# Kernel optimization log

Measured on AMD Instinct MI355X. Metric: run time of the kernel, lower is better.

The kernel has to match this reference:

```python
import math
import jax, jax.numpy as jnp
import numpy as np

B, S, D, H, M, R = 4, 2048, 512, 8, 4, 32
HD = D // H
EPS = 1e-8


def setup_inputs() -> dict:
    key = jax.random.key(0)
    ks = jax.random.split(key, 12)
    sc = 1.0 / math.sqrt(D)
    return {
        "x": jax.random.normal(ks[0], (B, S, D), jnp.float32),
        "Wq": jax.random.normal(ks[1], (D, D), jnp.float32) * sc,
        "bq": jnp.zeros((D,), jnp.float32),
        "Wk": jax.random.normal(ks[2], (D, D), jnp.float32) * sc,
        "bk": jnp.zeros((D,), jnp.float32),
        "Wv": jax.random.normal(ks[3], (D, D), jnp.float32) * sc,
        "bv": jnp.zeros((D,), jnp.float32),
        "mask1": jax.random.normal(ks[4], (M, R, S), jnp.float32) * (1.0 / math.sqrt(R)),
        "mask2": jax.random.normal(ks[5], (M, R, S), jnp.float32) * (1.0 / math.sqrt(R)),
        "Wo": jax.random.normal(ks[6], (D, D), jnp.float32) * sc,
        "bo": jnp.zeros((D,), jnp.float32),
        "roll_back": jax.random.randint(ks[7], (1, S, S), 0, S, jnp.int32),
    }


def reference(x, Wq, bq, Wk, bk, Wv, bv, mask1, mask2, Wo, bo, roll_back):
    # q, k, v: [B, H, S, HD]  (torch Linear: x @ W.T + b)
    def proj(W, b):
        return (x @ W.T + b).reshape(B, S, H, HD).transpose(0, 2, 1, 3)
    q, k, v = proj(Wq, bq), proj(Wk, bk), proj(Wv, bv)

    # learnable_mask[m,s,t] = sum_r mask1[m,r,s] * mask2[m,r,t]  -> [M, S, S]
    lm = jnp.einsum("mrs,mrt->mst", mask1, mask2)
    # gather along last dim with roll indices expanded to [M, S, S]
    idx = jnp.broadcast_to(roll_back, lm.shape)
    lm_rolled = jnp.take_along_axis(lm, idx, axis=-1)  # [M, S, S]

    # att: [B, H, S, S]
    att = jnp.einsum("bhsd,bhtd->bhst", q, k) / math.sqrt(HD)
    # group heads: [B, H/M, M, S, S] * [1, 1, M, S, S]
    att = att.reshape(B, H // M, M, S, S) * lm_rolled[None, None]
    att = att.reshape(B, H, S, S)

    # Frobenius norm over last two dims, per (batch, head)
    fro = jnp.sqrt(jnp.sum(att * att, axis=(-2, -1), keepdims=True))
    att = att / (fro + EPS)

    out = jnp.einsum("bhst,bhtd->bshd", att, v).reshape(B, S, D)
    return out @ Wo.T + bo
```

## Files before the change

### kernel.cpp

```cpp
#include <hip/hip_runtime.h>
#include <hip/hip_bf16.h>

#define NB 4
#define NS 2048
#define ND 512
#define NH 8
#define NM 4
#define NR 32
#define NHD 64

typedef short frag_ab __attribute__((ext_vector_type(8)));
typedef float frag_cd __attribute__((ext_vector_type(4)));

__device__ __forceinline__ float bf2f(short s) {
    union { unsigned u; float f; } c;
    c.u = ((unsigned)(unsigned short)s) << 16;
    return c.f;
}
__device__ __forceinline__ short f2bf(float f) {
    __hip_bfloat16 h = __float2bfloat16(f);
    union { __hip_bfloat16 h; short s; } c;
    c.h = h;
    return c.s;
}

__device__ __forceinline__ void gload16(const void* g, void* l) {
    __builtin_amdgcn_global_load_lds((const __attribute__((address_space(1))) unsigned int*)g,
                                     (__attribute__((address_space(3))) unsigned int*)l,
                                     16, 0, 0);
}

__device__ __forceinline__ void stage_tile(const short* src, size_t srcStride,
                                           char* lbase, int slot) {
    int o = slot * 16;
    int row = o >> 7;
    int cc = ((o >> 4) & 7) ^ (row & 7);
    gload16(src + (size_t)row * srcStride + cc * 8, lbase + o);
}

__device__ __forceinline__ frag_ab lds_frag(const char* lbase, int row, int cc_un) {
    int cc = cc_un ^ (row & 7);
    return *(const frag_ab*)(lbase + row * 128 + cc * 16);
}

__global__ void __launch_bounds__(256) k_cast(const float* __restrict__ in,
                                              short* __restrict__ out, int n8) {
    int i = blockIdx.x * 256 + threadIdx.x;
    if (i >= n8) return;
    const float4* p = (const float4*)in + (size_t)i * 2;
    float4 a = p[0], b = p[1];
    frag_ab o;
    o[0] = f2bf(a.x); o[1] = f2bf(a.y); o[2] = f2bf(a.z); o[3] = f2bf(a.w);
    o[4] = f2bf(b.x); o[5] = f2bf(b.y); o[6] = f2bf(b.z); o[7] = f2bf(b.w);
    ((frag_ab*)out)[i] = o;
}

__global__ void __launch_bounds__(256) k_tcast_mask(const float* __restrict__ in,
                                                    short* __restrict__ out) {
    int m = blockIdx.y, s0 = blockIdx.x * 64, tid = threadIdx.x;
    __shared__ float tile[32][65];
    int c = tid & 63, r4 = tid >> 6;
#pragma unroll
    for (int p = 0; p < 8; ++p) {
        int r = p * 4 + r4;
        tile[r][c] = in[(m * 32 + r) * NS + s0 + c];
    }
    __syncthreads();
    int r = tid & 31, s4 = tid >> 5;
#pragma unroll
    for (int p = 0; p < 8; ++p) {
        int s = p * 8 + s4;
        out[(m * NS + s0 + s) * NR + r] = f2bf(tile[r][s]);
    }
}

__global__ void __launch_bounds__(64) k_lm(const short* __restrict__ m1t,
                                           const short* __restrict__ m2t,
                                           short* __restrict__ lm) {
    int tb = blockIdx.x * 64, sb = blockIdx.y * 64, m = blockIdx.z;
    int lane = threadIdx.x;
    int lo = lane & 15, g = lane >> 4;
    frag_ab a[4], b[4];
#pragma unroll
    for (int i = 0; i < 4; ++i) {
        a[i] = *(const frag_ab*)(m1t + (m * NS + sb + i * 16 + lo) * NR + g * 8);
        b[i] = *(const frag_ab*)(m2t + (m * NS + tb + i * 16 + lo) * NR + g * 8);
    }
#pragma unroll
    for (int mi = 0; mi < 4; ++mi)
#pragma unroll
        for (int ni = 0; ni < 4; ++ni) {
            frag_cd z = {0.f, 0.f, 0.f, 0.f};
            frag_cd d = __builtin_amdgcn_mfma_f32_16x16x32_bf16(a[mi], b[ni], z, 0, 0, 0);
#pragma unroll
            for (int r = 0; r < 4; ++r) {
                int srow = sb + mi * 16 + g * 4 + r;
                int tcol = tb + ni * 16 + lo;
                lm[(size_t)(m * NS + srow) * NS + tcol] = f2bf(d[r]);
            }
        }
}

__global__ void __launch_bounds__(256) k_roll(const short* __restrict__ lm,
                                              const int* __restrict__ roll,
                                              short* __restrict__ lmr) {
    int bid = blockIdx.x;
    int m = bid & 3, s = bid >> 2;
    __shared__ __align__(16) short row[NS];
    int tid = threadIdx.x;
    size_t base = (size_t)(m * NS + s) * NS;
    *(frag_ab*)(row + tid * 8) = *(const frag_ab*)(lm + base + tid * 8);
    __syncthreads();
    const int* rrow = roll + (size_t)s * NS;
#pragma unroll
    for (int k = 0; k < 8; ++k) {
        int t = k * 256 + tid;
        lmr[base + t] = row[rrow[t]];
    }
}

template <int MODE>
__global__ void __launch_bounds__(256) k_gemm(const short* __restrict__ A,
                                              const short* __restrict__ W,
                                              const float* __restrict__ bias,
                                              void* __restrict__ out) {
    int n = blockIdx.x;
    int Mb = (n & 7) * 8 + ((n >> 3) & 7);
    int Nb = n >> 6;
    int bm0 = Mb * 128, bn0 = Nb * 128;
    int tid = threadIdx.x;
    int wid = tid >> 6, lane = tid & 63;
    int lo = lane & 15, g = lane >> 4;
    int wr = (wid >> 1) * 64, wc = (wid & 1) * 64;

    __shared__ __align__(16) char sm[2][32768];

    frag_cd acc[4][4];
#pragma unroll
    for (int mi = 0; mi < 4; ++mi)
#pragma unroll
        for (int ni = 0; ni < 4; ++ni) acc[mi][ni] = (frag_cd){0.f, 0.f, 0.f, 0.f};

    const short* Abase = A + (size_t)bm0 * ND;
    const short* Wbase = W + (size_t)bn0 * ND;

#pragma unroll
    for (int j = 0; j < 4; ++j) stage_tile(Abase, ND, sm[0], tid + j * 256);
#pragma unroll
    for (int j = 0; j < 4; ++j) stage_tile(Wbase, ND, sm[0] + 16384, tid + j * 256);
    __syncthreads();

    char* cb = sm[0];
    char* nb = sm[1];
    for (int kt = 0; kt < 8; ++kt) {
        if (kt < 7) {
            int k0 = (kt + 1) * 64;
#pragma unroll
            for (int j = 0; j < 4; ++j) stage_tile(Abase + k0, ND, nb, tid + j * 256);
#pragma unroll
            for (int j = 0; j < 4; ++j) stage_tile(Wbase + k0, ND, nb + 16384, tid + j * 256);
        }
#pragma unroll
        for (int kk = 0; kk < 2; ++kk) {
            frag_ab af[4], bf[4];
#pragma unroll
            for (int mi = 0; mi < 4; ++mi) af[mi] = lds_frag(cb, wr + mi * 16 + lo, kk * 4 + g);
#pragma unroll
            for (int ni = 0; ni < 4; ++ni) bf[ni] = lds_frag(cb + 16384, wc + ni * 16 + lo, kk * 4 + g);
#pragma unroll
            for (int mi = 0; mi < 4; ++mi)
#pragma unroll
                for (int ni = 0; ni < 4; ++ni)
                    acc[mi][ni] = __builtin_amdgcn_mfma_f32_16x16x32_bf16(af[mi], bf[ni], acc[mi][ni], 0, 0, 0);
        }
        __syncthreads();
        char* t = cb; cb = nb; nb = t;
    }

#pragma unroll
    for (int mi = 0; mi < 4; ++mi)
#pragma unroll
        for (int ni = 0; ni < 4; ++ni)
#pragma unroll
            for (int r = 0; r < 4; ++r) {
                int row = bm0 + wr + mi * 16 + g * 4 + r;
                int col = bn0 + wc + ni * 16 + lo;
                float v = acc[mi][ni][r] + bias[col];
                int b = row >> 11, s = row & 2047, h = col >> 6, d = col & 63;
                if (MODE == 0) {
                    ((short*)out)[(((size_t)(b * NH + h) * NS + s) << 6) + d] = f2bf(v);
                } else if (MODE == 1) {
                    ((short*)out)[((size_t)(b * NH + h) * NHD + d) * NS + s] = f2bf(v);
                } else {
                    ((float*)out)[(size_t)row * ND + col] = v;
                }
            }
}

__global__ void __launch_bounds__(512) k_attn(const short* __restrict__ Qb,
                                              const short* __restrict__ Kb,
                                              const short* __restrict__ Vt,
                                              const short* __restrict__ lmr,
                                              short* __restrict__ O,
                                              float* __restrict__ fro) {
    int n = blockIdx.x;
    int h = n & 7;
    int slot = n >> 3;
    int b = slot >> 4;
    int sb = slot & 15;
    int bh = b * NH + h;
    int m = h & 3;
    int tid = threadIdx.x;
    int w = tid >> 6, lane = tid & 63;
    int lo = lane & 15, g = lane >> 4;
    int srow = sb * 128 + w * 16;

    __shared__ __align__(16) char kv[2][16384];
    __shared__ __align__(16) short plds[8][1024];
    char* pbase = (char*)&plds[w][0];

    const short* kbase = Kb + (size_t)bh * NS * NHD;
    const short* vbase = Vt + (size_t)bh * NHD * NS;
    const short* lmbase = lmr + ((size_t)m * NS + srow + lo) * NS;

    const short* qptr = Qb + ((size_t)bh * NS + srow + lo) * NHD + g * 8;
    frag_ab qf[2];
    qf[0] = *(const frag_ab*)(qptr);
    qf[1] = *(const frag_ab*)(qptr + 32);

    frag_cd acco[4];
#pragma unroll
    for (int ni = 0; ni < 4; ++ni) acco[ni] = (frag_cd){0.f, 0.f, 0.f, 0.f};
    float sumsq = 0.f;

    stage_tile(kbase, NHD, kv[0], tid);
    stage_tile(vbase, NS, kv[0] + 8192, tid);
    __syncthreads();

    char* cb = kv[0];
    char* nb = kv[1];
    for (int tb = 0; tb < 32; ++tb) {
        int t0 = tb * 64;
        if (tb < 31) {
            stage_tile(kbase + (size_t)(t0 + 64) * NHD, NHD, nb, tid);
            stage_tile(vbase + (t0 + 64), NS, nb + 8192, tid);
        }
        frag_cd sacc[4];
#pragma unroll
        for (int ni = 0; ni < 4; ++ni) sacc[ni] = (frag_cd){0.f, 0.f, 0.f, 0.f};
#pragma unroll
        for (int kk = 0; kk < 2; ++kk)
#pragma unroll
            for (int ni = 0; ni < 4; ++ni)
                sacc[ni] = __builtin_amdgcn_mfma_f32_16x16x32_bf16(
                    qf[kk], lds_frag(cb, ni * 16 + lo, kk * 4 + g), sacc[ni], 0, 0, 0);
#pragma unroll
        for (int ni = 0; ni < 4; ++ni)
#pragma unroll
            for (int r = 0; r < 4; ++r) {
                int rs = g * 4 + r;
                int ct = ni * 16 + lo;
                int byte = (rs * 128 + ct * 2) ^ ((rs & 7) << 4);
                *(short*)(pbase + byte) = f2bf(sacc[ni][r]);
            }
        frag_ab pf[2];
#pragma unroll
        for (int kk = 0; kk < 2; ++kk) {
            int rbyte = (lo * 128 + kk * 64 + g * 16) ^ ((lo & 7) << 4);
            frag_ab sf = *(const frag_ab*)(pbase + rbyte);
            frag_ab lf = *(const frag_ab*)(lmbase + t0 + kk * 32 + g * 8);
            frag_ab pp;
#pragma unroll
            for (int j = 0; j < 8; ++j) {
                float p = bf2f(sf[j]) * bf2f(lf[j]) * 0.125f;
                sumsq += p * p;
                pp[j] = f2bf(p);
            }
            pf[kk] = pp;
        }
#pragma unroll
        for (int ni = 0; ni < 4; ++ni)
#pragma unroll
            for (int kk = 0; kk < 2; ++kk)
                acco[ni] = __builtin_amdgcn_mfma_f32_16x16x32_bf16(
                    pf[kk], lds_frag(cb + 8192, ni * 16 + lo, kk * 4 + g), acco[ni], 0, 0, 0);
        __syncthreads();
        char* t = cb; cb = nb; nb = t;
    }
#pragma unroll
    for (int off = 32; off; off >>= 1) sumsq += __shfl_xor(sumsq, off, 64);
    if (lane == 0) atomicAdd(&fro[bh], sumsq);
#pragma unroll
    for (int ni = 0; ni < 4; ++ni)
#pragma unroll
        for (int r = 0; r < 4; ++r) {
            int s = srow + g * 4 + r;
            int d = ni * 16 + lo;
            O[((size_t)(b * NS + s)) * ND + h * NHD + d] = f2bf(acco[ni][r]);
        }
}

__global__ void k_fro(const float* __restrict__ fro, float* __restrict__ inv) {
    int i = threadIdx.x;
    if (i < NB * NH) inv[i] = 1.f / (sqrtf(fro[i]) + 1e-8f);
}

__global__ void __launch_bounds__(256) k_scale(short* __restrict__ O,
                                               const float* __restrict__ inv) {
    int i = blockIdx.x * 256 + threadIdx.x;
    int i8 = i * 8;
    int col = i8 & 511;
    int row = i8 >> 9;
    float sc = inv[(row >> 11) * NH + (col >> 6)];
    frag_ab v = ((frag_ab*)O)[i];
    frag_ab o;
#pragma unroll
    for (int j = 0; j < 8; ++j) o[j] = f2bf(bf2f(v[j]) * sc);
    ((frag_ab*)O)[i] = o;
}

extern "C" void kernel_launch(void* const* d_in, const int* in_sizes, int n_in,
                              void* d_out, int out_size, void* d_ws, size_t ws_size,
                              hipStream_t stream) {
    const float* x     = (const float*)d_in[0];
    const float* Wq    = (const float*)d_in[1];
    const float* bq    = (const float*)d_in[2];
    const float* Wk    = (const float*)d_in[3];
    const float* bk    = (const float*)d_in[4];
    const float* Wv    = (const float*)d_in[5];
    const float* bv    = (const float*)d_in[6];
    const float* mask1 = (const float*)d_in[7];
    const float* mask2 = (const float*)d_in[8];
    const float* Wo    = (const float*)d_in[9];
    const float* bo    = (const float*)d_in[10];
    const int*   roll  = (const int*)d_in[11];
    float* out = (float*)d_out;

    char* ws = (char*)d_ws;
    short* xb  = (short*)(ws + 0);
    short* Wqb = (short*)(ws + 8388608);
    short* Wkb = (short*)(ws + 8912896);
    short* Wvb = (short*)(ws + 9437184);
    short* Wob = (short*)(ws + 9961472);
    short* Qb  = (short*)(ws + 10485760);
    short* Kb  = (short*)(ws + 18874368);
    short* Vtb = (short*)(ws + 27262976);
    short* m1t = (short*)(ws + 35651584);
    short* m2t = (short*)(ws + 36175872);
    short* lm  = (short*)(ws + 36700160);
    short* lmr = (short*)(ws + 70254592);
    short* Ob  = (short*)(ws + 103809024);
    float* fro = (float*)(ws + 112197632);
    float* inv = (float*)(ws + 112197760);

    k_cast<<<2048, 256, 0, stream>>>(x, xb, (NB * NS * ND) / 8);
    k_cast<<<128, 256, 0, stream>>>(Wq, Wqb, (ND * ND) / 8);
    k_cast<<<128, 256, 0, stream>>>(Wk, Wkb, (ND * ND) / 8);
    k_cast<<<128, 256, 0, stream>>>(Wv, Wvb, (ND * ND) / 8);
    k_cast<<<128, 256, 0, stream>>>(Wo, Wob, (ND * ND) / 8);
    k_tcast_mask<<<dim3(32, 4), 256, 0, stream>>>(mask1, m1t);
    k_tcast_mask<<<dim3(32, 4), 256, 0, stream>>>(mask2, m2t);

    k_lm<<<dim3(32, 32, 4), 64, 0, stream>>>(m1t, m2t, lm);
    k_roll<<<8192, 256, 0, stream>>>(lm, roll, lmr);

    k_gemm<0><<<256, 256, 0, stream>>>(xb, Wqb, bq, Qb);
    k_gemm<0><<<256, 256, 0, stream>>>(xb, Wkb, bk, Kb);
    k_gemm<1><<<256, 256, 0, stream>>>(xb, Wvb, bv, Vtb);

    hipMemsetAsync(fro, 0, 128, stream);
    k_attn<<<512, 512, 0, stream>>>(Qb, Kb, Vtb, lmr, Ob, fro);

    k_fro<<<1, 64, 0, stream>>>(fro, inv);
    k_scale<<<2048, 256, 0, stream>>>(Ob, inv);
    k_gemm<2><<<256, 256, 0, stream>>>(Ob, Wob, bo, out);
}
```

Before: 285.8 us.

## Merge launches, fuse QKV GEMMs, vectorize roll gather, prefetch mask, remap attention blocks

Measured after the change: 252.9 us. 11.5% less time.

```diff
diff --git a/kernel.cpp b/kernel.cpp
--- a/kernel.cpp
+++ b/kernel.cpp
@@ -55,9 +55,32 @@
     ((frag_ab*)out)[i] = o;
 }
 
-__global__ void __launch_bounds__(256) k_tcast_mask(const float* __restrict__ in,
-                                                    short* __restrict__ out) {
-    int m = blockIdx.y, s0 = blockIdx.x * 64, tid = threadIdx.x;
+__global__ void __launch_bounds__(256) k_castw(const float* __restrict__ Wq,
+                                               const float* __restrict__ Wk,
+                                               const float* __restrict__ Wv,
+                                               const float* __restrict__ Wo,
+                                               short* __restrict__ out) {
+    int i = blockIdx.x * 256 + threadIdx.x;
+    int which = i >> 15;
+    int j = i & 32767;
+    const float* src = which == 0 ? Wq : which == 1 ? Wk : which == 2 ? Wv : Wo;
+    const float4* p = (const float4*)src + (size_t)j * 2;
+    float4 a = p[0], b = p[1];
+    frag_ab o;
+    o[0] = f2bf(a.x); o[1] = f2bf(a.y); o[2] = f2bf(a.z); o[3] = f2bf(a.w);
+    o[4] = f2bf(b.x); o[5] = f2bf(b.y); o[6] = f2bf(b.z); o[7] = f2bf(b.w);
+    ((frag_ab*)out)[i] = o;
+}
+
+__global__ void __launch_bounds__(256) k_tcast_mask(const float* __restrict__ mask1,
+                                                    const float* __restrict__ mask2,
+                                                    short* __restrict__ m1t,
+                                                    short* __restrict__ m2t) {
+    int my = blockIdx.y;
+    const float* in = my < 4 ? mask1 : mask2;
+    short* out = my < 4 ? m1t : m2t;
+    int m = my & 3;
+    int s0 = blockIdx.x * 64, tid = threadIdx.x;
     __shared__ float tile[32][65];
     int c = tid & 63, r4 = tid >> 6;
 #pragma unroll
@@ -112,34 +135,47 @@
     *(frag_ab*)(row + tid * 8) = *(const frag_ab*)(lm + base + tid * 8);
     __syncthreads();
     const int* rrow = roll + (size_t)s * NS;
-#pragma unroll
-    for (int k = 0; k < 8; ++k) {
-        int t = k * 256 + tid;
-        lmr[base + t] = row[rrow[t]];
-    }
-}
-
-template <int MODE>
-__global__ void __launch_bounds__(256) k_gemm(const short* __restrict__ A,
-                                              const short* __restrict__ W,
-                                              const float* __restrict__ bias,
-                                              void* __restrict__ out) {
+    int t0 = tid * 8;
+    int4 r0 = *(const int4*)(rrow + t0);
+    int4 r1 = *(const int4*)(rrow + t0 + 4);
+    frag_ab o;
+    o[0] = row[r0.x]; o[1] = row[r0.y]; o[2] = row[r0.z]; o[3] = row[r0.w];
+    o[4] = row[r1.x]; o[5] = row[r1.y]; o[6] = row[r1.z]; o[7] = row[r1.w];
+    *(frag_ab*)(lmr + base + t0) = o;
+}
+
+__global__ void __launch_bounds__(256) k_gemm_qkv(const short* __restrict__ A,
+                                                  const short* __restrict__ Wqb,
+                                                  const short* __restrict__ Wkb,
+                                                  const short* __restrict__ Wvb,
+                                                  const float* __restrict__ bq,
+                                                  const float* __restrict__ bk,
+                                                  const float* __restrict__ bv,
+                                                  short* __restrict__ Qb,
+                                                  short* __restrict__ Kb,
+                                                  short* __restrict__ Vtb) {
     int n = blockIdx.x;
-    int Mb = (n & 7) * 8 + ((n >> 3) & 7);
-    int Nb = n >> 6;
-    int bm0 = Mb * 128, bn0 = Nb * 128;
+    int rr = n >> 3;
+    int Mb = (n & 7) * 8 + (rr & 7);
+    int Nb = rr >> 3;
+    int which = Nb >> 3;
+    int bn0 = (Nb & 7) * 64;
+    const short* W = which == 0 ? Wqb : which == 1 ? Wkb : Wvb;
+    const float* bias = which == 0 ? bq : which == 1 ? bk : bv;
+    short* out = which == 0 ? Qb : which == 1 ? Kb : Vtb;
+    int bm0 = Mb * 128;
     int tid = threadIdx.x;
     int wid = tid >> 6, lane = tid & 63;
     int lo = lane & 15, g = lane >> 4;
-    int wr = (wid >> 1) * 64, wc = (wid & 1) * 64;
-
-    __shared__ __align__(16) char sm[2][32768];
-
-    frag_cd acc[4][4];
+    int wr = (wid >> 1) * 64, wc = (wid & 1) * 32;
+
+    __shared__ __align__(16) char sm[2][24576];
+
+    frag_cd acc[4][2];
 #pragma unroll
     for (int mi = 0; mi < 4; ++mi)
 #pragma unroll
-        for (int ni = 0; ni < 4; ++ni) acc[mi][ni] = (frag_cd){0.f, 0.f, 0.f, 0.f};
+        for (int ni = 0; ni < 2; ++ni) acc[mi][ni] = (frag_cd){0.f, 0.f, 0.f, 0.f};
 
     const short* Abase = A + (size_t)bm0 * ND;
     const short* Wbase = W + (size_t)bn0 * ND;
@@ -147,7 +183,7 @@
 #pragma unroll
     for (int j = 0; j < 4; ++j) stage_tile(Abase, ND, sm[0], tid + j * 256);
 #pragma unroll
-    for (int j = 0; j < 4; ++j) stage_tile(Wbase, ND, sm[0] + 16384, tid + j * 256);
+    for (int j = 0; j < 2; ++j) stage_tile(Wbase, ND, sm[0] + 16384, tid + j * 256);
     __syncthreads();
 
     char* cb = sm[0];
@@ -158,19 +194,19 @@
 #pragma unroll
             for (int j = 0; j < 4; ++j) stage_tile(Abase + k0, ND, nb, tid + j * 256);
 #pragma unroll
-            for (int j = 0; j < 4; ++j) stage_tile(Wbase + k0, ND, nb + 16384, tid + j * 256);
+            for (int j = 0; j < 2; ++j) stage_tile(Wbase + k0, ND, nb + 16384, tid + j * 256);
         }
 #pragma unroll
         for (int kk = 0; kk < 2; ++kk) {
-            frag_ab af[4], bf[4];
+            frag_ab af[4], bf[2];
 #pragma unroll
             for (int mi = 0; mi < 4; ++mi) af[mi] = lds_frag(cb, wr + mi * 16 + lo, kk * 4 + g);
 #pragma unroll
-            for (int ni = 0; ni < 4; ++ni) bf[ni] = lds_frag(cb + 16384, wc + ni * 16 + lo, kk * 4 + g);
+            for (int ni = 0; ni < 2; ++ni) bf[ni] = lds_frag(cb + 16384, wc + ni * 16 + lo, kk * 4 + g);
 #pragma unroll
             for (int mi = 0; mi < 4; ++mi)
 #pragma unroll
-                for (int ni = 0; ni < 4; ++ni)
+                for (int ni = 0; ni < 2; ++ni)
                     acc[mi][ni] = __builtin_amdgcn_mfma_f32_16x16x32_bf16(af[mi], bf[ni], acc[mi][ni], 0, 0, 0);
         }
         __syncthreads();
@@ -180,20 +216,89 @@
 #pragma unroll
     for (int mi = 0; mi < 4; ++mi)
 #pragma unroll
-        for (int ni = 0; ni < 4; ++ni)
-#pragma unroll
-            for (int r = 0; r < 4; ++r) {
-                int row = bm0 + wr + mi * 16 + g * 4 + r;
+        for (int ni = 0; ni < 2; ++ni)
+#pragma unroll
+            for (int ri = 0; ri < 4; ++ri) {
+                int row = bm0 + wr + mi * 16 + g * 4 + ri;
                 int col = bn0 + wc + ni * 16 + lo;
-                float v = acc[mi][ni][r] + bias[col];
+                float v = acc[mi][ni][ri] + bias[col];
                 int b = row >> 11, s = row & 2047, h = col >> 6, d = col & 63;
-                if (MODE == 0) {
-                    ((short*)out)[(((size_t)(b * NH + h) * NS + s) << 6) + d] = f2bf(v);
-                } else if (MODE == 1) {
-                    ((short*)out)[((size_t)(b * NH + h) * NHD + d) * NS + s] = f2bf(v);
+                if (which < 2) {
+                    out[(((size_t)(b * NH + h) * NS + s) << 6) + d] = f2bf(v);
                 } else {
-                    ((float*)out)[(size_t)row * ND + col] = v;
+                    out[((size_t)(b * NH + h) * NHD + d) * NS + s] = f2bf(v);
                 }
+            }
+}
+
+__global__ void __launch_bounds__(256) k_gemm_out(const short* __restrict__ A,
+                                                  const short* __restrict__ W,
+                                                  const float* __restrict__ bias,
+                                                  float* __restrict__ out) {
+    int n = blockIdx.x;
+    int rr = n >> 3;
+    int Mb = (n & 7) * 8 + (rr & 7);
+    int Nb = rr >> 3;
+    int bn0 = Nb * 64;
+    int bm0 = Mb * 128;
+    int tid = threadIdx.x;
+    int wid = tid >> 6, lane = tid & 63;
+    int lo = lane & 15, g = lane >> 4;
+    int wr = (wid >> 1) * 64, wc = (wid & 1) * 32;
+
+    __shared__ __align__(16) char sm[2][24576];
+
+    frag_cd acc[4][2];
+#pragma unroll
+    for (int mi = 0; mi < 4; ++mi)
+#pragma unroll
+        for (int ni = 0; ni < 2; ++ni) acc[mi][ni] = (frag_cd){0.f, 0.f, 0.f, 0.f};
+
+    const short* Abase = A + (size_t)bm0 * ND;
+    const short* Wbase = W + (size_t)bn0 * ND;
+
+#pragma unroll
+    for (int j = 0; j < 4; ++j) stage_tile(Abase, ND, sm[0], tid + j * 256);
+#pragma unroll
+    for (int j = 0; j < 2; ++j) stage_tile(Wbase, ND, sm[0] + 16384, tid + j * 256);
+    __syncthreads();
+
+    char* cb = sm[0];
+    char* nb = sm[1];
+    for (int kt = 0; kt < 8; ++kt) {
+        if (kt < 7) {
+            int k0 = (kt + 1) * 64;
+#pragma unroll
+            for (int j = 0; j < 4; ++j) stage_tile(Abase + k0, ND, nb, tid + j * 256);
+#pragma unroll
+            for (int j = 0; j < 2; ++j) stage_tile(Wbase + k0, ND, nb + 16384, tid + j * 256);
+        }
+#pragma unroll
+        for (int kk = 0; kk < 2; ++kk) {
+            frag_ab af[4], bf[2];
+#pragma unroll
+            for (int mi = 0; mi < 4; ++mi) af[mi] = lds_frag(cb, wr + mi * 16 + lo, kk * 4 + g);
+#pragma unroll
+            for (int ni = 0; ni < 2; ++ni) bf[ni] = lds_frag(cb + 16384, wc + ni * 16 + lo, kk * 4 + g);
+#pragma unroll
+            for (int mi = 0; mi < 4; ++mi)
+#pragma unroll
+                for (int ni = 0; ni < 2; ++ni)
+                    acc[mi][ni] = __builtin_amdgcn_mfma_f32_16x16x32_bf16(af[mi], bf[ni], acc[mi][ni], 0, 0, 0);
+        }
+        __syncthreads();
+        char* t = cb; cb = nb; nb = t;
+    }
+
+#pragma unroll
+    for (int mi = 0; mi < 4; ++mi)
+#pragma unroll
+        for (int ni = 0; ni < 2; ++ni)
+#pragma unroll
+            for (int ri = 0; ri < 4; ++ri) {
+                int row = bm0 + wr + mi * 16 + g * 4 + ri;
+                int col = bn0 + wc + ni * 16 + lo;
+                out[(size_t)row * ND + col] = acc[mi][ni][ri] + bias[col];
             }
 }
 
@@ -204,12 +309,15 @@
                                               short* __restrict__ O,
                                               float* __restrict__ fro) {
     int n = blockIdx.x;
-    int h = n & 7;
-    int slot = n >> 3;
-    int b = slot >> 4;
-    int sb = slot & 15;
+    int xcd = n & 7;
+    int idx = n >> 3;
+    int b = idx & 3;
+    int hh = (idx >> 2) & 1;
+    int sbl = idx >> 3;
+    int m = xcd >> 1;
+    int sb = (xcd & 1) * 8 + sbl;
+    int h = hh * 4 + m;
     int bh = b * NH + h;
-    int m = h & 3;
     int tid = threadIdx.x;
     int w = tid >> 6, lane = tid & 63;
     int lo = lane & 15, g = lane >> 4;
@@ -235,15 +343,20 @@
 
     stage_tile(kbase, NHD, kv[0], tid);
     stage_tile(vbase, NS, kv[0] + 8192, tid);
+    frag_ab lc0 = *(const frag_ab*)(lmbase + g * 8);
+    frag_ab lc1 = *(const frag_ab*)(lmbase + 32 + g * 8);
     __syncthreads();
 
     char* cb = kv[0];
     char* nb = kv[1];
     for (int tb = 0; tb < 32; ++tb) {
         int t0 = tb * 64;
+        frag_ab ln0 = lc0, ln1 = lc1;
         if (tb < 31) {
             stage_tile(kbase + (size_t)(t0 + 64) * NHD, NHD, nb, tid);
             stage_tile(vbase + (t0 + 64), NS, nb + 8192, tid);
+            ln0 = *(const frag_ab*)(lmbase + t0 + 64 + g * 8);
+            ln1 = *(const frag_ab*)(lmbase + t0 + 96 + g * 8);
         }
         frag_cd sacc[4];
 #pragma unroll
@@ -268,7 +381,7 @@
         for (int kk = 0; kk < 2; ++kk) {
             int rbyte = (lo * 128 + kk * 64 + g * 16) ^ ((lo & 7) << 4);
             frag_ab sf = *(const frag_ab*)(pbase + rbyte);
-            frag_ab lf = *(const frag_ab*)(lmbase + t0 + kk * 32 + g * 8);
+            frag_ab lf = kk ? lc1 : lc0;
             frag_ab pp;
 #pragma unroll
             for (int j = 0; j < 8; ++j) {
@@ -284,6 +397,8 @@
             for (int kk = 0; kk < 2; ++kk)
                 acco[ni] = __builtin_amdgcn_mfma_f32_16x16x32_bf16(
                     pf[kk], lds_frag(cb + 8192, ni * 16 + lo, kk * 4 + g), acco[ni], 0, 0, 0);
+        lc0 = ln0;
+        lc1 = ln1;
         __syncthreads();
         char* t = cb; cb = nb; nb = t;
     }
@@ -300,18 +415,14 @@
         }
 }
 
-__global__ void k_fro(const float* __restrict__ fro, float* __restrict__ inv) {
-    int i = threadIdx.x;
-    if (i < NB * NH) inv[i] = 1.f / (sqrtf(fro[i]) + 1e-8f);
-}
-
 __global__ void __launch_bounds__(256) k_scale(short* __restrict__ O,
-                                               const float* __restrict__ inv) {
+                                               const float* __restrict__ fro) {
     int i = blockIdx.x * 256 + threadIdx.x;
     int i8 = i * 8;
     int col = i8 & 511;
     int row = i8 >> 9;
-    float sc = inv[(row >> 11) * NH + (col >> 6)];
+    float f = fro[(row >> 11) * NH + (col >> 6)];
+    float sc = 1.f / (sqrtf(f) + 1e-8f);
     frag_ab v = ((frag_ab*)O)[i];
     frag_ab o;
 #pragma unroll
@@ -351,27 +462,19 @@
     short* lmr = (short*)(ws + 70254592);
     short* Ob  = (short*)(ws + 103809024);
     float* fro = (float*)(ws + 112197632);
-    float* inv = (float*)(ws + 112197760);
 
     k_cast<<<2048, 256, 0, stream>>>(x, xb, (NB * NS * ND) / 8);
-    k_cast<<<128, 256, 0, stream>>>(Wq, Wqb, (ND * ND) / 8);
-    k_cast<<<128, 256, 0, stream>>>(Wk, Wkb, (ND * ND) / 8);
-    k_cast<<<128, 256, 0, stream>>>(Wv, Wvb, (ND * ND) / 8);
-    k_cast<<<128, 256, 0, stream>>>(Wo, Wob, (ND * ND) / 8);
-    k_tcast_mask<<<dim3(32, 4), 256, 0, stream>>>(mask1, m1t);
-    k_tcast_mask<<<dim3(32, 4), 256, 0, stream>>>(mask2, m2t);
+    k_castw<<<512, 256, 0, stream>>>(Wq, Wk, Wv, Wo, Wqb);
+    k_tcast_mask<<<dim3(32, 8), 256, 0, stream>>>(mask1, mask2, m1t, m2t);
 
     k_lm<<<dim3(32, 32, 4), 64, 0, stream>>>(m1t, m2t, lm);
     k_roll<<<8192, 256, 0, stream>>>(lm, roll, lmr);
 
-    k_gemm<0><<<256, 256, 0, stream>>>(xb, Wqb, bq, Qb);
-    k_gemm<0><<<256, 256, 0, stream>>>(xb, Wkb, bk, Kb);
-    k_gemm<1><<<256, 256, 0, stream>>>(xb, Wvb, bv, Vtb);
+    k_gemm_qkv<<<1536, 256, 0, stream>>>(xb, Wqb, Wkb, Wvb, bq, bk, bv, Qb, Kb, Vtb);
 
     hipMemsetAsync(fro, 0, 128, stream);
     k_attn<<<512, 512, 0, stream>>>(Qb, Kb, Vtb, lmr, Ob, fro);
 
-    k_fro<<<1, 64, 0, stream>>>(fro, inv);
-    k_scale<<<2048, 256, 0, stream>>>(Ob, inv);
-    k_gemm<2><<<256, 256, 0, stream>>>(Ob, Wob, bo, out);
-}
+    k_scale<<<2048, 256, 0, stream>>>(Ob, fro);
+    k_gemm_out<<<512, 256, 0, stream>>>(Ob, Wob, bo, out);
+}
```
